# Performance work log

Hardware: AMD Instinct MI355X
Metric: run time of the kernel (lower is better)

The kernel has to match this reference:

```python
import jax, jax.numpy as jnp
import numpy as np
from jax import lax

B, D, S, H, W, T = 128, 512, 30, 14, 14, 12


def setup_inputs() -> dict:
    key = jax.random.key(0)
    ks = jax.random.split(key, 28)
    f = lambda k, shape: jax.random.normal(k, shape, jnp.float32) * 0.05
    return {
        "q": f(ks[0], (B, D)),
        "cws": f(ks[1], (B, D, S)),
        "KB": f(ks[2], (B, D, H, W)),
        "c0": f(ks[3], (B, D)),
        "m0": f(ks[4], (B, D)),
        "Wq": f(ks[5], (D, D)), "bq": f(ks[6], (D,)),
        "Wct": f(ks[7], (2 * D, D)), "bct": f(ks[8], (D,)),
        "wca": f(ks[9], (D,)), "bca": f(ks[10], ()),
        "Wm": f(ks[11], (D, D)), "bm": f(ks[12], (D,)),
        "Wkb": f(ks[13], (D, D)), "bkb": f(ks[14], (D,)),
        "Wrm": f(ks[15], (2 * D, D)), "brm": f(ks[16], (D,)),
        "wra": f(ks[17], (D,)), "bra": f(ks[18], ()),
        "Wwm": f(ks[19], (2 * D, D)), "bwm": f(ks[20], (D,)),
        "wwa": f(ks[21], (D,)), "bwa": f(ks[22], ()),
        "Wam": f(ks[23], (2 * D, D)), "bam": f(ks[24], (D,)),
        "Wg": f(ks[25], (D, D)), "bg": f(ks[26], (D,)),
        "steps": T,
    }


def _mac(q, cws, KB, c0, m0, Wq, bq, Wct, bct, wca, bca, Wm, bm, Wkb, bkb,
         Wrm, brm, wra, bra, Wwm, bwm, wwa, bwa, Wam, bam, Wg, bg, steps):
    b, d, h, w = KB.shape[0], KB.shape[1], KB.shape[2], KB.shape[3]
    KBp = jnp.transpose(KB, (0, 2, 3, 1))          # B,H,W,d
    KB2 = KBp @ Wkb + bkb                           # KB_transform (step-invariant)
    q_i = q @ Wq + bq                               # q_transform (step-invariant)

    nhist = steps + 1
    c_hist = jnp.zeros((nhist, b, d), KB.dtype).at[0].set(c0)
    m_hist = jnp.zeros((nhist, b, d), KB.dtype).at[0].set(m0)

    def step(carry, t):
        c_hist, m_hist, c_prev, m_prev = carry
        # ---- ControlUnit ----
        cq = jnp.concatenate([q_i, c_prev], axis=-1) @ Wct + bct   # B,d
        clog = jnp.einsum('bds,d->bs', cq[:, :, None] * cws, wca) + bca
        cattn = jax.nn.softmax(clog, axis=-1)                       # B,S
        c_i = jnp.einsum('bs,bds->bd', cattn, cws)
        # ---- ReadUnit ----
        mp = m_prev @ Wm + bm                                       # B,d
        I = mp[:, None, None, :] * KB2                              # B,H,W,d
        Im = jnp.concatenate([I, KBp], axis=-1) @ Wrm + brm         # B,H,W,d
        rlog = jnp.einsum('bhwd,d->bhw', c_i[:, None, None, :] * Im, wra) + bra
        rattn = jax.nn.softmax(rlog.reshape(b, -1), axis=-1).reshape(b, h, w)
        m_new = jnp.einsum('bhw,bhwd->bd', rattn, KBp)
        # ---- WriteUnit (self_attn + mem_gate) ----
        _m = jnp.concatenate([m_new, m_prev], axis=-1) @ Wwm + bwm
        slog = jnp.einsum('tbd,d->bt', c_i[None] * c_hist, wwa) + bwa
        valid = jnp.arange(nhist) <= t
        slog = jnp.where(valid[None, :], slog, jnp.float32(-1e9))
        sattn = jax.nn.softmax(slog, axis=-1)                       # B,T+1
        m_sa = jnp.einsum('bt,tbd->bd', sattn, m_hist)
        _m = jnp.concatenate([m_sa, _m], axis=-1) @ Wam + bam
        g = jax.nn.sigmoid(c_i @ Wg + bg)
        _m = g * m_prev + (1.0 - g) * _m
        c_hist = c_hist.at[t + 1].set(c_i)
        m_hist = m_hist.at[t + 1].set(_m)
        return (c_hist, m_hist, c_i, _m), None

    (c_hist, m_hist, c_last, m_last), _ = lax.scan(
        step, (c_hist, m_hist, c0, m0), jnp.arange(steps))
    return m_last


def reference(q, cws, KB, c0, m0, Wq, bq, Wct, bct, wca, bca, Wm, bm, Wkb, bkb,
              Wrm, brm, wra, bra, Wwm, bwm, wwa, bwa, Wam, bam, Wg, bg, steps):
    return _mac(q, cws, KB, c0, m0, Wq, bq, Wct, bct, wca, bca, Wm, bm, Wkb, bkb,
                Wrm, brm, wra, bra, Wwm, bwm, wwa, bwa, Wam, bam, Wg, bg, steps)
```

## Files before the change

kernel.cpp:

```cpp
#include <hip/hip_runtime.h>
#include <cstdint>

#define BB 128
#define DD 512
#define SS 30
#define PP 196
#define TT 12
#define BD (BB*DD)

typedef unsigned short ushortT;
typedef unsigned int uintT;

__device__ __forceinline__ float bf2f(ushortT u)
{
    return __uint_as_float(((uintT)u) << 16);
}

struct GDesc {
    const float *A0, *A1;
    const float *W0, *W1;
    const float *bias;
    float *out;
    const float *e1;
    int nparts, epi, mblk, nblk, aux;
};
struct GPack { GDesc d[6]; };

__global__ __launch_bounds__(256)
void gemm4(GPack pk)
{
    GDesc d = pk.d[blockIdx.z];
    if ((int)blockIdx.x >= d.mblk || (int)blockIdx.y >= d.nblk) return;
    const int tid  = threadIdx.x;
    const int lane = tid & 63;
    const int wv   = __builtin_amdgcn_readfirstlane(tid >> 6);

    if (d.epi == 5) {
        int b = blockIdx.x * 4 + blockIdx.y;
        const float* sat = d.W0 + b * 16;
        float a0 = 0.f, a1 = 0.f;
        for (int tp = 0; tp <= d.aux; ++tp) {
            float s = sat[tp];
            const float* mh = d.A0 + (size_t)tp * BD + (size_t)b * DD;
            a0 = fmaf(s, mh[tid], a0);
            a1 = fmaf(s, mh[tid + 256], a1);
        }
        d.out[(size_t)b * DD + tid] = a0;
        d.out[(size_t)b * DD + tid + 256] = a1;
        return;
    }

    const int m0 = blockIdx.x * 4;
    const int c0 = blockIdx.y * 128;
    float accx[4], accy[4];
    #pragma unroll
    for (int m = 0; m < 4; ++m) { accx[m] = 0.f; accy[m] = 0.f; }

    for (int p = 0; p < d.nparts; ++p) {
        const float* A = p ? d.A1 : d.A0;
        const float* W = p ? d.W1 : d.W0;
        const float* a = A + (size_t)m0 * 512 + wv * 128;
        const float2* Wb = (const float2*)(W + (size_t)(wv * 128) * 512 + c0) + lane;
        #pragma unroll 4
        for (int k = 0; k < 128; ++k) {
            float2 w2 = Wb[(size_t)k * 256];
            #pragma unroll
            for (int m = 0; m < 4; ++m) {
                float av = a[m * 512 + k];
                accx[m] = fmaf(av, w2.x, accx[m]);
                accy[m] = fmaf(av, w2.y, accy[m]);
            }
        }
    }

    __shared__ float red[4][4][128];
    #pragma unroll
    for (int m = 0; m < 4; ++m)
        *(float2*)&red[wv][m][lane * 2] = make_float2(accx[m], accy[m]);
    __syncthreads();

    for (int i = tid; i < 512; i += 256) {
        int mm = i >> 7, cl = i & 127;
        float s = (red[0][mm][cl] + red[1][mm][cl])
                + (red[2][mm][cl] + red[3][mm][cl]);
        int row = m0 + mm, col = c0 + cl;
        size_t o = (size_t)row * 512 + col;
        if (d.epi == 0)      d.out[o] = s + d.bias[col];
        else if (d.epi == 1) { float v = s + d.bias[col];
                               d.out[o] = 1.f / (1.f + __expf(-v)); }
        else if (d.epi == 4) d.out[o] = s + d.e1[o];
        else                 d.out[o] = s;
    }
}

struct SP {
    const float *cq, *cws, *cwsT, *wca, *bca, *wra, *wwa, *bwa;
    float *c_hist, *sattn, *vb;
    const float *msa, *mnw, *gb, *b2, *Wam, *WA, *WB;
    float *m_hist, *dst;
    int t;
};

__global__ __launch_bounds__(512)
void stepA(SP P)
{
    const int tid = threadIdx.x;
    const int lane = tid & 63;
    __shared__ float cqw[512], ciw[512];
    __shared__ float clog2[32], cattn[32], slog[16];
    __shared__ float red[8][2][128];

    if ((int)blockIdx.x < 128) {
        if (P.t >= TT) return;
        int b = blockIdx.x, w = tid >> 6, t = P.t;
        cqw[tid] = P.cq[(size_t)b*DD + tid] * P.wca[tid];
        __syncthreads();
        for (int s = w; s < SS; s += 8) {
            const float* row = P.cwsT + ((size_t)b*SS + s)*DD;
            float a = 0.f;
            #pragma unroll
            for (int j = 0; j < 8; ++j)
                a = fmaf(cqw[lane + 64*j], row[lane + 64*j], a);
            for (int off = 32; off; off >>= 1) a += __shfl_xor(a, off, 64);
            if (lane == 0) clog2[s] = a;
        }
        __syncthreads();
        if (tid < 32) {
            float v = (tid < SS) ? clog2[tid] + P.bca[0] : -1e30f;
            float mx = v;
            for (int off = 16; off; off >>= 1) mx = fmaxf(mx, __shfl_xor(mx, off, 32));
            float e = (tid < SS) ? __expf(v - mx) : 0.f;
            float sm = e;
            for (int off = 16; off; off >>= 1) sm += __shfl_xor(sm, off, 32);
            cattn[tid] = e / sm;
        }
        __syncthreads();
        {
            const float* base = P.cws + (size_t)b*DD*SS + (size_t)tid*SS;
            float acc = 0.f;
            #pragma unroll
            for (int j = 0; j < SS; ++j) acc = fmaf(cattn[j], base[j], acc);
            P.c_hist[(size_t)(t+1)*BD + (size_t)b*DD + tid] = acc;
            P.vb[(size_t)b*DD + tid] = acc * P.wra[tid];
            ciw[tid] = acc * P.wwa[tid];
        }
        __syncthreads();
        for (int tp = tid >> 6; tp <= t; tp += 8) {
            const float* ch = P.c_hist + (size_t)tp*BD + (size_t)b*DD;
            float a = 0.f;
            #pragma unroll
            for (int j = 0; j < 8; ++j)
                a = fmaf(ciw[lane + 64*j], ch[lane + 64*j], a);
            for (int off = 32; off; off >>= 1) a += __shfl_xor(a, off, 64);
            if (lane == 0) slog[tp] = a;
        }
        __syncthreads();
        if (tid < 16) {
            float v = (tid <= t) ? slog[tid] + P.bwa[0] : -1e30f;
            float mx = v;
            for (int off = 8; off; off >>= 1) mx = fmaxf(mx, __shfl_xor(mx, off, 16));
            float e = (tid <= t) ? __expf(v - mx) : 0.f;
            float sm = e;
            for (int off = 8; off; off >>= 1) sm += __shfl_xor(sm, off, 16);
            P.sattn[b*16 + tid] = e / sm;
        }
    } else {
        if (P.t == 0) return;
        int gb_ = blockIdx.x - 128;
        int mt = gb_ >> 2, nc = gb_ & 3;
        int wv = __builtin_amdgcn_readfirstlane(tid >> 6);
        const int koff = wv * 64;
        const float* mprev = P.m_hist + (size_t)(P.t - 1) * BD;
        const int r0 = mt * 2;
        float ax0 = 0.f, ay0 = 0.f, ax1 = 0.f, ay1 = 0.f;

        {
            const float* a = P.msa + (size_t)r0 * 512 + koff;
            const float2* Wb = (const float2*)(P.Wam + (size_t)koff * 512 + nc * 128) + lane;
            #pragma unroll 8
            for (int k = 0; k < 64; ++k) {
                float2 w2 = Wb[(size_t)k * 256];
                float av0 = a[k], av1 = a[512 + k];
                ax0 = fmaf(av0, w2.x, ax0); ay0 = fmaf(av0, w2.y, ay0);
                ax1 = fmaf(av1, w2.x, ax1); ay1 = fmaf(av1, w2.y, ay1);
            }
        }
        {
            const float* a = P.mnw + (size_t)r0 * 512 + koff;
            const float2* Wb = (const float2*)(P.WA + (size_t)koff * 512 + nc * 128) + lane;
            #pragma unroll 8
            for (int k = 0; k < 64; ++k) {
                float2 w2 = Wb[(size_t)k * 256];
                float av0 = a[k], av1 = a[512 + k];
                ax0 = fmaf(av0, w2.x, ax0); ay0 = fmaf(av0, w2.y, ay0);
                ax1 = fmaf(av1, w2.x, ax1); ay1 = fmaf(av1, w2.y, ay1);
            }
        }
        {
            const float* a = mprev + (size_t)r0 * 512 + koff;
            const float2* Wb = (const float2*)(P.WB + (size_t)koff * 512 + nc * 128) + lane;
            #pragma unroll 8
            for (int k = 0; k < 64; ++k) {
                float2 w2 = Wb[(size_t)k * 256];
                float av0 = a[k], av1 = a[512 + k];
                ax0 = fmaf(av0, w2.x, ax0); ay0 = fmaf(av0, w2.y, ay0);
                ax1 = fmaf(av1, w2.x, ax1); ay1 = fmaf(av1, w2.y, ay1);
            }
        }
        *(float2*)&red[wv][0][lane*2] = make_float2(ax0, ay0);
        *(float2*)&red[wv][1][lane*2] = make_float2(ax1, ay1);
        __syncthreads();
        if (tid < 256) {
            int mm = tid >> 7, cl = tid & 127;
            float s = 0.f;
            #pragma unroll
            for (int j = 0; j < 8; ++j) s += red[j][mm][cl];
            int row = r0 + mm, col = nc*128 + cl;
            size_t o = (size_t)row*512 + col;
            float v = s + P.b2[col];
            float g = P.gb[o];
            float pv = mprev[o];
            P.dst[o] = g*pv + (1.f - g)*v;
        }
    }
}

__global__ __launch_bounds__(256)
void read1y(const ushortT* __restrict__ KBh, const float* __restrict__ ubuf,
            const float* __restrict__ mp, const float* __restrict__ WkbT,
            const float* __restrict__ vW, float* __restrict__ rlogp)
{
    int b = blockIdx.x, dg = blockIdx.y, tid = threadIdx.x;
    int lane = tid & 63, w = tid >> 6;
    __shared__ float red[4][64];
    __shared__ float yb[64];
    {
        const float* ur = ubuf + (size_t)b*512;
        const float* mr = mp + (size_t)b*512;
        const float* Wc = WkbT + dg*64 + lane;
        float s = 0.f;
        for (int k = w*128; k < w*128 + 128; ++k)
            s = fmaf(ur[k]*mr[k], Wc[(size_t)k*512], s);
        red[w][lane] = s;
    }
    __syncthreads();
    if (tid < 64)
        yb[tid] = (red[0][tid]+red[1][tid]) + (red[2][tid]+red[3][tid])
                + vW[(size_t)b*512 + dg*64 + tid];
    __syncthreads();
    float a0=0.f, a1=0.f, a2=0.f, a3=0.f;
    if (tid < PP) {
        const ushortT* kb = KBh + ((size_t)b*512 + dg*64)*PP + tid;
        #pragma unroll 4
        for (int dd = 0; dd < 64; dd += 4) {
            a0 = fmaf(bf2f(kb[(size_t)(dd+0)*PP]), yb[dd+0], a0);
            a1 = fmaf(bf2f(kb[(size_t)(dd+1)*PP]), yb[dd+1], a1);
            a2 = fmaf(bf2f(kb[(size_t)(dd+2)*PP]), yb[dd+2], a2);
            a3 = fmaf(bf2f(kb[(size_t)(dd+3)*PP]), yb[dd+3], a3);
        }
    }
    rlogp[((size_t)b*8 + dg)*256 + tid] = (a0+a1)+(a2+a3);
}

__global__ __launch_bounds__(256)
void read2(const ushortT* __restrict__ KBh, const float* __restrict__ rlogp,
           float* __restrict__ m_new)
{
    int b = blockIdx.x, dg = blockIdx.y;
    int tid = threadIdx.x, lane = tid & 63, w = tid >> 6;
    __shared__ float ex[256];
    __shared__ float wred[4];

    float v = -1e30f;
    if (tid < PP) {
        const float* rp = rlogp + (size_t)b*2048 + tid;
        float t0 = rp[0]    + rp[256];
        float t1 = rp[512]  + rp[768];
        float t2 = rp[1024] + rp[1280];
        float t3 = rp[1536] + rp[1792];
        v = (t0+t1)+(t2+t3);
    }
    float mx = v;
    for (int off = 32; off; off >>= 1) mx = fmaxf(mx, __shfl_xor(mx, off, 64));
    if (lane == 0) wred[w] = mx;
    __syncthreads();
    float gmax = fmaxf(fmaxf(wred[0], wred[1]), fmaxf(wred[2], wred[3]));
    float e = (tid < PP) ? __expf(v - gmax) : 0.f;
    float sm = e;
    for (int off = 32; off; off >>= 1) sm += __shfl_xor(sm, off, 64);
    __syncthreads();
    if (lane == 0) wred[w] = sm;
    __syncthreads();
    float inv = 1.f / ((wred[0]+wred[1]) + (wred[2]+wred[3]));
    ex[tid] = e * inv;
    __syncthreads();

    #pragma unroll 2
    for (int i = 0; i < 16; ++i) {
        int d = dg*64 + w*16 + i;
        const ushortT* row = KBh + ((size_t)b*512 + d)*PP;
        float a = ex[lane]       * bf2f(row[lane])
                + ex[lane + 64]  * bf2f(row[lane + 64])
                + ex[lane + 128] * bf2f(row[lane + 128]);
        if (lane < PP - 192) a = fmaf(ex[lane + 192], bf2f(row[lane + 192]), a);
        for (int off = 32; off; off >>= 1) a += __shfl_xor(a, off, 64);
        if (lane == 0) m_new[(size_t)b*512 + d] = a;
    }
}

__global__ __launch_bounds__(256)
void transpose3(const float* __restrict__ Wrm, const float* __restrict__ Wkb,
                float* __restrict__ WrmTu, float* __restrict__ WrmTv,
                float* __restrict__ WkbT)
{
    const float* src = (blockIdx.z == 0) ? Wrm
                     : (blockIdx.z == 1) ? (Wrm + 512*512) : Wkb;
    float* dst = (blockIdx.z == 0) ? WrmTu : (blockIdx.z == 1) ? WrmTv : WkbT;
    __shared__ float tile[32][33];
    int bx = blockIdx.x*32, by = blockIdx.y*32;
    int tx = threadIdx.x & 31, ty = threadIdx.x >> 5;
    #pragma unroll
    for (int i = 0; i < 32; i += 8)
        tile[ty+i][tx] = src[(size_t)(by+ty+i)*512 + bx+tx];
    __syncthreads();
    #pragma unroll
    for (int i = 0; i < 32; i += 8)
        dst[(size_t)(bx+ty+i)*512 + by+tx] = tile[tx][ty+i];
}

__global__ __launch_bounds__(256)
void transpose_cws(const float* __restrict__ cws, float* __restrict__ cwsT)
{
    int b = blockIdx.x, dc = blockIdx.y;
    __shared__ float tile[32][33];
    int tid = threadIdx.x;
    const float* src = cws + ((size_t)b*DD + dc*32) * SS;
    for (int i = tid; i < 1024; i += 256) {
        int r = i >> 5, s = i & 31;
        if (s < SS) tile[r][s] = src[(size_t)r*SS + s];
    }
    __syncthreads();
    for (int i = tid; i < 1024; i += 256) {
        int s = i >> 5, r = i & 31;
        if (s < SS)
            cwsT[((size_t)b*SS + s)*DD + dc*32 + r] = tile[r][s];
    }
}

__global__ __launch_bounds__(256)
void kb_convert(const float* __restrict__ KB, ushortT* __restrict__ KBh)
{
    size_t i = ((size_t)blockIdx.x * 256 + threadIdx.x) * 8;
    #pragma unroll
    for (int j = 0; j < 8; ++j) {
        uintT bits = __float_as_uint(KB[i + j]);
        uintT r = (bits + 0x7FFFu + ((bits >> 16) & 1u)) >> 16;
        KBh[i + j] = (ushortT)r;
    }
}

__global__ __launch_bounds__(256)
void vecmat(const float* __restrict__ v, const float* __restrict__ W,
            const float* __restrict__ bias, float* __restrict__ out)
{
    int lane = threadIdx.x & 63, w = threadIdx.x >> 6;
    int n = blockIdx.x * 64 + lane;
    float s = 0.f;
    for (int k = w*128; k < w*128 + 128; ++k)
        s = fmaf(v[k], W[(size_t)k*512 + n], s);
    __shared__ float red[4][64];
    red[w][lane] = s;
    __syncthreads();
    if (threadIdx.x < 64) {
        int nn = blockIdx.x * 64 + threadIdx.x;
        out[nn] = red[0][threadIdx.x] + red[1][threadIdx.x]
                + red[2][threadIdx.x] + red[3][threadIdx.x] + bias[nn];
    }
}

__global__ __launch_bounds__(256)
void init_hist(const float* __restrict__ c0, const float* __restrict__ m0,
               float* __restrict__ c_hist, float* __restrict__ m_hist)
{
    int i = blockIdx.x * 256 + threadIdx.x;
    if (i < BD) { c_hist[i] = c0[i]; m_hist[i] = m0[i]; }
}

extern "C" void kernel_launch(void* const* d_in, const int* in_sizes, int n_in,
                              void* d_out, int out_size, void* d_ws, size_t ws_size,
                              hipStream_t stream)
{
    (void)in_sizes; (void)n_in; (void)out_size; (void)ws_size;
    const float* q   = (const float*)d_in[0];
    const float* cws = (const float*)d_in[1];
    const float* KB  = (const float*)d_in[2];
    const float* c0  = (const float*)d_in[3];
    const float* m0  = (const float*)d_in[4];
    const float* Wq  = (const float*)d_in[5];
    const float* bq  = (const float*)d_in[6];
    const float* Wct = (const float*)d_in[7];
    const float* bct = (const float*)d_in[8];
    const float* wca = (const float*)d_in[9];
    const float* bca = (const float*)d_in[10];
    const float* Wm  = (const float*)d_in[11];
    const float* bm  = (const float*)d_in[12];
    const float* Wkb = (const float*)d_in[13];
    const float* Wrm = (const float*)d_in[15];
    const float* wra = (const float*)d_in[17];
    const float* Wwm = (const float*)d_in[19];
    const float* bwm = (const float*)d_in[20];
    const float* wwa = (const float*)d_in[21];
    const float* bwa = (const float*)d_in[22];
    const float* Wam = (const float*)d_in[23];
    const float* bam = (const float*)d_in[24];
    const float* Wg  = (const float*)d_in[25];
    const float* bg  = (const float*)d_in[26];

    float* ws      = (float*)d_ws;
    float* c_hist  = ws;
    float* m_hist  = ws + 13*BD;
    float* qct     = ws + 26*BD;
    float* q_i     = ws + 27*BD;
    float* cq      = ws + 28*BD;
    float* mp      = ws + 29*BD;
    float* vb      = ws + 30*BD;
    float* ubuf    = ws + 31*BD;
    float* vW      = ws + 32*BD;
    float* gb      = ws + 33*BD;
    float* msa     = ws + 34*BD;
    float* mnw     = ws + 35*BD;
    float* sattn   = ws + 36*BD;
    float* rlogp   = ws + 37*BD;
    float* WrmTu   = ws + 41*BD;
    float* WrmTv   = ws + 45*BD;
    float* WkbT    = ws + 49*BD;
    float* WA      = ws + 53*BD;
    float* WB      = ws + 57*BD;
    float* b2      = ws + 61*BD;
    float* cwsT    = ws + 62*BD;
    ushortT* KBh   = (ushortT*)(ws + 92*BD);

    const float* Wct_bot = Wct + 512*512;
    const float* Wam_bot = Wam + 512*512;
    const float* Wwm_bot = Wwm + 512*512;
    dim3 blk(256);
    GDesc Z = { nullptr,nullptr,nullptr,nullptr,nullptr,nullptr,nullptr,
                1, 6, 0, 0, 0 };

    transpose3<<<dim3(16,16,3), blk, 0, stream>>>(Wrm, Wkb, WrmTu, WrmTv, WkbT);
    transpose_cws<<<dim3(128,16), blk, 0, stream>>>(cws, cwsT);
    kb_convert<<<dim3(6272), blk, 0, stream>>>(KB, KBh);
    init_hist<<<dim3(BD/256), blk, 0, stream>>>(c0, m0, c_hist, m_hist);
    {
        GPack pk;
        pk.d[0] = { Wwm, nullptr, Wam_bot, nullptr, nullptr, WA, nullptr,
                    1, 6, 128, 4, 0 };
        pk.d[1] = { Wwm_bot, nullptr, Wam_bot, nullptr, nullptr, WB, nullptr,
                    1, 6, 128, 4, 0 };
        pk.d[2] = { q, nullptr, Wq, nullptr, bq, q_i, nullptr,
                    1, 0, 32, 4, 0 };
        pk.d[3] = Z; pk.d[4] = Z; pk.d[5] = Z;
        gemm4<<<dim3(128,4,3), blk, 0, stream>>>(pk);
    }
    {
        GPack pk;
        pk.d[0] = { q_i, nullptr, Wct, nullptr, bct, qct, nullptr,
                    1, 0, 32, 4, 0 };
        pk.d[1] = { q_i, c0, Wct, Wct_bot, bct, cq, nullptr,
                    2, 0, 32, 4, 0 };
        pk.d[2] = Z; pk.d[3] = Z; pk.d[4] = Z; pk.d[5] = Z;
        gemm4<<<dim3(32,4,2), blk, 0, stream>>>(pk);
    }
    vecmat<<<dim3(8), blk, 0, stream>>>(bwm, Wam_bot, bam, b2);

    for (int t = 0; t <= TT; ++t) {
        {
            SP P;
            P.cq = cq; P.cws = cws; P.cwsT = cwsT;
            P.wca = wca; P.bca = bca; P.wra = wra; P.wwa = wwa; P.bwa = bwa;
            P.c_hist = c_hist; P.sattn = sattn; P.vb = vb;
            P.msa = msa; P.mnw = mnw; P.gb = gb; P.b2 = b2;
            P.Wam = Wam; P.WA = WA; P.WB = WB;
            P.m_hist = m_hist;
            P.dst = (t == TT) ? (float*)d_out : (m_hist + (size_t)t * BD);
            P.t = t;
            stepA<<<dim3(384), dim3(512), 0, stream>>>(P);
        }
        if (t == TT) break;

        float* c_i = c_hist + (size_t)(t+1) * BD;
        {
            GPack pk;
            pk.d[0] = { vb, nullptr, WrmTu, nullptr, nullptr, ubuf, nullptr,
                        1, 6, 32, 4, 0 };
            pk.d[1] = { vb, nullptr, WrmTv, nullptr, nullptr, vW, nullptr,
                        1, 6, 32, 4, 0 };
            pk.d[2] = { c_i, nullptr, Wg, nullptr, bg, gb, nullptr,
                        1, 1, 32, 4, 0 };
            pk.d[3] = { c_i, nullptr, Wct_bot, nullptr, nullptr, cq, qct,
                        1, 4, 32, 4, 0 };
            pk.d[4] = { m_hist + (size_t)t * BD, nullptr, Wm, nullptr, bm, mp,
                        nullptr, 1, 0, 32, 4, 0 };
            pk.d[5] = { m_hist, nullptr, sattn, nullptr, nullptr, msa, nullptr,
                        1, 5, 32, 4, t };
            gemm4<<<dim3(32,4,6), blk, 0, stream>>>(pk);
        }
        read1y<<<dim3(BB,8), blk, 0, stream>>>(KBh, ubuf, mp, WkbT, vW, rlogp);
        read2<<<dim3(BB,8), blk, 0, stream>>>(KBh, rlogp, mnw);
    }
}
```

Measured before the change: 793.8 us.

## Fuse read kernels with grid barrier, merge setup kernels, widen GEMM row tiles

Merges read1y and read2 into one kernel that waits on a per-batch atomic counter, so each batch's 8 blocks can reach the softmax/read phase without a second launch. Folds the setup kernels (transposes, bf16 conversion, history init, bias vecmat) into a single launch. Doubles rows per block in gemm4 and stepA's GEMM path, halving grid sizes and improving weight reuse. The trade-offs are fewer blocks and less parallelism, plus the spin-wait, which relies on all 8 blocks of a batch being co-resident to avoid deadlock.

```diff
diff --git a/kernel.cpp b/kernel.cpp
--- a/kernel.cpp
+++ b/kernel.cpp
@@ -36,25 +36,28 @@
     const int wv   = __builtin_amdgcn_readfirstlane(tid >> 6);
 
     if (d.epi == 5) {
-        int b = blockIdx.x * 4 + blockIdx.y;
-        const float* sat = d.W0 + b * 16;
-        float a0 = 0.f, a1 = 0.f;
-        for (int tp = 0; tp <= d.aux; ++tp) {
-            float s = sat[tp];
-            const float* mh = d.A0 + (size_t)tp * BD + (size_t)b * DD;
-            a0 = fmaf(s, mh[tid], a0);
-            a1 = fmaf(s, mh[tid + 256], a1);
-        }
-        d.out[(size_t)b * DD + tid] = a0;
-        d.out[(size_t)b * DD + tid + 256] = a1;
+        int bb = (blockIdx.x * 4 + blockIdx.y) * 2;
+        #pragma unroll
+        for (int b = bb; b < bb + 2; ++b) {
+            const float* sat = d.W0 + b * 16;
+            float a0 = 0.f, a1 = 0.f;
+            for (int tp = 0; tp <= d.aux; ++tp) {
+                float s = sat[tp];
+                const float* mh = d.A0 + (size_t)tp * BD + (size_t)b * DD;
+                a0 = fmaf(s, mh[tid], a0);
+                a1 = fmaf(s, mh[tid + 256], a1);
+            }
+            d.out[(size_t)b * DD + tid] = a0;
+            d.out[(size_t)b * DD + tid + 256] = a1;
+        }
         return;
     }
 
-    const int m0 = blockIdx.x * 4;
+    const int m0 = blockIdx.x * 8;
     const int c0 = blockIdx.y * 128;
-    float accx[4], accy[4];
+    float accx[8], accy[8];
     #pragma unroll
-    for (int m = 0; m < 4; ++m) { accx[m] = 0.f; accy[m] = 0.f; }
+    for (int m = 0; m < 8; ++m) { accx[m] = 0.f; accy[m] = 0.f; }
 
     for (int p = 0; p < d.nparts; ++p) {
         const float* A = p ? d.A1 : d.A0;
@@ -65,7 +68,7 @@
         for (int k = 0; k < 128; ++k) {
             float2 w2 = Wb[(size_t)k * 256];
             #pragma unroll
-            for (int m = 0; m < 4; ++m) {
+            for (int m = 0; m < 8; ++m) {
                 float av = a[m * 512 + k];
                 accx[m] = fmaf(av, w2.x, accx[m]);
                 accy[m] = fmaf(av, w2.y, accy[m]);
@@ -73,13 +76,13 @@
         }
     }
 
-    __shared__ float red[4][4][128];
+    __shared__ float red[4][8][128];
     #pragma unroll
-    for (int m = 0; m < 4; ++m)
+    for (int m = 0; m < 8; ++m)
         *(float2*)&red[wv][m][lane * 2] = make_float2(accx[m], accy[m]);
     __syncthreads();
 
-    for (int i = tid; i < 512; i += 256) {
+    for (int i = tid; i < 1024; i += 256) {
         int mm = i >> 7, cl = i & 127;
         float s = (red[0][mm][cl] + red[1][mm][cl])
                 + (red[2][mm][cl] + red[3][mm][cl]);
@@ -108,7 +111,7 @@
     const int lane = tid & 63;
     __shared__ float cqw[512], ciw[512];
     __shared__ float clog2[32], cattn[32], slog[16];
-    __shared__ float red[8][2][128];
+    __shared__ float red[8][4][128];
 
     if ((int)blockIdx.x < 128) {
         if (P.t >= TT) return;
@@ -171,46 +174,53 @@
         int wv = __builtin_amdgcn_readfirstlane(tid >> 6);
         const int koff = wv * 64;
         const float* mprev = P.m_hist + (size_t)(P.t - 1) * BD;
-        const int r0 = mt * 2;
-        float ax0 = 0.f, ay0 = 0.f, ax1 = 0.f, ay1 = 0.f;
+        const int r0 = mt * 4;
+        float ax[4] = {0.f,0.f,0.f,0.f}, ay[4] = {0.f,0.f,0.f,0.f};
 
         {
             const float* a = P.msa + (size_t)r0 * 512 + koff;
             const float2* Wb = (const float2*)(P.Wam + (size_t)koff * 512 + nc * 128) + lane;
-            #pragma unroll 8
+            #pragma unroll 4
             for (int k = 0; k < 64; ++k) {
                 float2 w2 = Wb[(size_t)k * 256];
-                float av0 = a[k], av1 = a[512 + k];
-                ax0 = fmaf(av0, w2.x, ax0); ay0 = fmaf(av0, w2.y, ay0);
-                ax1 = fmaf(av1, w2.x, ax1); ay1 = fmaf(av1, w2.y, ay1);
+                #pragma unroll
+                for (int m = 0; m < 4; ++m) {
+                    float av = a[m*512 + k];
+                    ax[m] = fmaf(av, w2.x, ax[m]); ay[m] = fmaf(av, w2.y, ay[m]);
+                }
             }
         }
         {
             const float* a = P.mnw + (size_t)r0 * 512 + koff;
             const float2* Wb = (const float2*)(P.WA + (size_t)koff * 512 + nc * 128) + lane;
-            #pragma unroll 8
+            #pragma unroll 4
             for (int k = 0; k < 64; ++k) {
                 float2 w2 = Wb[(size_t)k * 256];
-                float av0 = a[k], av1 = a[512 + k];
-                ax0 = fmaf(av0, w2.x, ax0); ay0 = fmaf(av0, w2.y, ay0);
-                ax1 = fmaf(av1, w2.x, ax1); ay1 = fmaf(av1, w2.y, ay1);
+                #pragma unroll
+                for (int m = 0; m < 4; ++m) {
+                    float av = a[m*512 + k];
+                    ax[m] = fmaf(av, w2.x, ax[m]); ay[m] = fmaf(av, w2.y, ay[m]);
+                }
             }
         }
         {
             const float* a = mprev + (size_t)r0 * 512 + koff;
             const float2* Wb = (const float2*)(P.WB + (size_t)koff * 512 + nc * 128) + lane;
-            #pragma unroll 8
+            #pragma unroll 4
             for (int k = 0; k < 64; ++k) {
                 float2 w2 = Wb[(size_t)k * 256];
-                float av0 = a[k], av1 = a[512 + k];
-                ax0 = fmaf(av0, w2.x, ax0); ay0 = fmaf(av0, w2.y, ay0);
-                ax1 = fmaf(av1, w2.x, ax1); ay1 = fmaf(av1, w2.y, ay1);
+                #pragma unroll
+                for (int m = 0; m < 4; ++m) {
+                    float av = a[m*512 + k];
+                    ax[m] = fmaf(av, w2.x, ax[m]); ay[m] = fmaf(av, w2.y, ay[m]);
+                }
             }
         }
-        *(float2*)&red[wv][0][lane*2] = make_float2(ax0, ay0);
-        *(float2*)&red[wv][1][lane*2] = make_float2(ax1, ay1);
-        __syncthreads();
-        if (tid < 256) {
+        #pragma unroll
+        for (int m = 0; m < 4; ++m)
+            *(float2*)&red[wv][m][lane*2] = make_float2(ax[m], ay[m]);
+        __syncthreads();
+        {
             int mm = tid >> 7, cl = tid & 127;
             float s = 0.f;
             #pragma unroll
@@ -226,14 +236,18 @@
 }
 
 __global__ __launch_bounds__(256)
-void read1y(const ushortT* __restrict__ KBh, const float* __restrict__ ubuf,
-            const float* __restrict__ mp, const float* __restrict__ WkbT,
-            const float* __restrict__ vW, float* __restrict__ rlogp)
+void readfused(const ushortT* __restrict__ KBh, const float* __restrict__ ubuf,
+               const float* __restrict__ mp, const float* __restrict__ WkbT,
+               const float* __restrict__ vW, float* __restrict__ rlogp,
+               float* __restrict__ m_new, int* __restrict__ rcnt, int t)
 {
     int b = blockIdx.x, dg = blockIdx.y, tid = threadIdx.x;
     int lane = tid & 63, w = tid >> 6;
     __shared__ float red[4][64];
     __shared__ float yb[64];
+    __shared__ float ex[256];
+    __shared__ float wred[4];
+
     {
         const float* ur = ubuf + (size_t)b*512;
         const float* mr = mp + (size_t)b*512;
@@ -248,28 +262,31 @@
         yb[tid] = (red[0][tid]+red[1][tid]) + (red[2][tid]+red[3][tid])
                 + vW[(size_t)b*512 + dg*64 + tid];
     __syncthreads();
-    float a0=0.f, a1=0.f, a2=0.f, a3=0.f;
-    if (tid < PP) {
-        const ushortT* kb = KBh + ((size_t)b*512 + dg*64)*PP + tid;
-        #pragma unroll 4
-        for (int dd = 0; dd < 64; dd += 4) {
-            a0 = fmaf(bf2f(kb[(size_t)(dd+0)*PP]), yb[dd+0], a0);
-            a1 = fmaf(bf2f(kb[(size_t)(dd+1)*PP]), yb[dd+1], a1);
-            a2 = fmaf(bf2f(kb[(size_t)(dd+2)*PP]), yb[dd+2], a2);
-            a3 = fmaf(bf2f(kb[(size_t)(dd+3)*PP]), yb[dd+3], a3);
-        }
-    }
-    rlogp[((size_t)b*8 + dg)*256 + tid] = (a0+a1)+(a2+a3);
-}
-
-__global__ __launch_bounds__(256)
-void read2(const ushortT* __restrict__ KBh, const float* __restrict__ rlogp,
-           float* __restrict__ m_new)
-{
-    int b = blockIdx.x, dg = blockIdx.y;
-    int tid = threadIdx.x, lane = tid & 63, w = tid >> 6;
-    __shared__ float ex[256];
-    __shared__ float wred[4];
+    {
+        float a0=0.f, a1=0.f, a2=0.f, a3=0.f;
+        if (tid < PP) {
+            const ushortT* kb = KBh + ((size_t)b*512 + dg*64)*PP + tid;
+            #pragma unroll 4
+            for (int dd = 0; dd < 64; dd += 4) {
+                a0 = fmaf(bf2f(kb[(size_t)(dd+0)*PP]), yb[dd+0], a0);
+                a1 = fmaf(bf2f(kb[(size_t)(dd+1)*PP]), yb[dd+1], a1);
+                a2 = fmaf(bf2f(kb[(size_t)(dd+2)*PP]), yb[dd+2], a2);
+                a3 = fmaf(bf2f(kb[(size_t)(dd+3)*PP]), yb[dd+3], a3);
+            }
+        }
+        rlogp[((size_t)b*8 + dg)*256 + tid] = (a0+a1)+(a2+a3);
+    }
+
+    __syncthreads();
+    if (tid == 0) {
+        int* c = rcnt + t*128 + b;
+        __threadfence();
+        __hip_atomic_fetch_add(c, 1, __ATOMIC_ACQ_REL, __HIP_MEMORY_SCOPE_AGENT);
+        while (__hip_atomic_load(c, __ATOMIC_ACQUIRE, __HIP_MEMORY_SCOPE_AGENT) < 8)
+            __builtin_amdgcn_s_sleep(2);
+        __threadfence();
+    }
+    __syncthreads();
 
     float v = -1e30f;
     if (tid < PP) {
@@ -308,82 +325,73 @@
     }
 }
 
+struct SetupP {
+    const float *Wrm, *Wkb, *cws, *KB, *c0v, *m0v, *bwm, *Wam_bot, *bam;
+    float *WrmTu, *WrmTv, *WkbT, *cwsT, *c_hist, *m_hist, *b2;
+    ushortT *KBh;
+};
+
 __global__ __launch_bounds__(256)
-void transpose3(const float* __restrict__ Wrm, const float* __restrict__ Wkb,
-                float* __restrict__ WrmTu, float* __restrict__ WrmTv,
-                float* __restrict__ WkbT)
+void setup_misc(SetupP P)
 {
-    const float* src = (blockIdx.z == 0) ? Wrm
-                     : (blockIdx.z == 1) ? (Wrm + 512*512) : Wkb;
-    float* dst = (blockIdx.z == 0) ? WrmTu : (blockIdx.z == 1) ? WrmTv : WkbT;
     __shared__ float tile[32][33];
-    int bx = blockIdx.x*32, by = blockIdx.y*32;
-    int tx = threadIdx.x & 31, ty = threadIdx.x >> 5;
-    #pragma unroll
-    for (int i = 0; i < 32; i += 8)
-        tile[ty+i][tx] = src[(size_t)(by+ty+i)*512 + bx+tx];
-    __syncthreads();
-    #pragma unroll
-    for (int i = 0; i < 32; i += 8)
-        dst[(size_t)(bx+ty+i)*512 + by+tx] = tile[tx][ty+i];
-}
-
-__global__ __launch_bounds__(256)
-void transpose_cws(const float* __restrict__ cws, float* __restrict__ cwsT)
-{
-    int b = blockIdx.x, dc = blockIdx.y;
-    __shared__ float tile[32][33];
-    int tid = threadIdx.x;
-    const float* src = cws + ((size_t)b*DD + dc*32) * SS;
-    for (int i = tid; i < 1024; i += 256) {
-        int r = i >> 5, s = i & 31;
-        if (s < SS) tile[r][s] = src[(size_t)r*SS + s];
-    }
-    __syncthreads();
-    for (int i = tid; i < 1024; i += 256) {
-        int s = i >> 5, r = i & 31;
-        if (s < SS)
-            cwsT[((size_t)b*SS + s)*DD + dc*32 + r] = tile[r][s];
-    }
-}
-
-__global__ __launch_bounds__(256)
-void kb_convert(const float* __restrict__ KB, ushortT* __restrict__ KBh)
-{
-    size_t i = ((size_t)blockIdx.x * 256 + threadIdx.x) * 8;
-    #pragma unroll
-    for (int j = 0; j < 8; ++j) {
-        uintT bits = __float_as_uint(KB[i + j]);
-        uintT r = (bits + 0x7FFFu + ((bits >> 16) & 1u)) >> 16;
-        KBh[i + j] = (ushortT)r;
-    }
-}
-
-__global__ __launch_bounds__(256)
-void vecmat(const float* __restrict__ v, const float* __restrict__ W,
-            const float* __restrict__ bias, float* __restrict__ out)
-{
-    int lane = threadIdx.x & 63, w = threadIdx.x >> 6;
-    int n = blockIdx.x * 64 + lane;
-    float s = 0.f;
-    for (int k = w*128; k < w*128 + 128; ++k)
-        s = fmaf(v[k], W[(size_t)k*512 + n], s);
-    __shared__ float red[4][64];
-    red[w][lane] = s;
-    __syncthreads();
-    if (threadIdx.x < 64) {
-        int nn = blockIdx.x * 64 + threadIdx.x;
-        out[nn] = red[0][threadIdx.x] + red[1][threadIdx.x]
-                + red[2][threadIdx.x] + red[3][threadIdx.x] + bias[nn];
-    }
-}
-
-__global__ __launch_bounds__(256)
-void init_hist(const float* __restrict__ c0, const float* __restrict__ m0,
-               float* __restrict__ c_hist, float* __restrict__ m_hist)
-{
-    int i = blockIdx.x * 256 + threadIdx.x;
-    if (i < BD) { c_hist[i] = c0[i]; m_hist[i] = m0[i]; }
+    int id = blockIdx.x, tid = threadIdx.x;
+
+    if (id < 768) {
+        int which = id >> 8, tj = id & 255;
+        const float* src = (which == 0) ? P.Wrm
+                         : (which == 1) ? (P.Wrm + 512*512) : P.Wkb;
+        float* dst = (which == 0) ? P.WrmTu : (which == 1) ? P.WrmTv : P.WkbT;
+        int bx = (tj & 15) * 32, by = (tj >> 4) * 32;
+        int tx = tid & 31, ty = tid >> 5;
+        #pragma unroll
+        for (int i = 0; i < 32; i += 8)
+            tile[ty+i][tx] = src[(size_t)(by+ty+i)*512 + bx+tx];
+        __syncthreads();
+        #pragma unroll
+        for (int i = 0; i < 32; i += 8)
+            dst[(size_t)(bx+ty+i)*512 + by+tx] = tile[tx][ty+i];
+    } else if (id < 2816) {
+        int j = id - 768;
+        int b = j >> 4, dc = j & 15;
+        const float* src = P.cws + ((size_t)b*DD + dc*32) * SS;
+        for (int i = tid; i < 1024; i += 256) {
+            int r = i >> 5, s = i & 31;
+            if (s < SS) tile[r][s] = src[(size_t)r*SS + s];
+        }
+        __syncthreads();
+        for (int i = tid; i < 1024; i += 256) {
+            int s = i >> 5, r = i & 31;
+            if (s < SS)
+                P.cwsT[((size_t)b*SS + s)*DD + dc*32 + r] = tile[r][s];
+        }
+    } else if (id < 9088) {
+        size_t i = ((size_t)(id - 2816) * 256 + tid) * 8;
+        #pragma unroll
+        for (int j = 0; j < 8; ++j) {
+            uintT bits = __float_as_uint(P.KB[i + j]);
+            uintT r = (bits + 0x7FFFu + ((bits >> 16) & 1u)) >> 16;
+            P.KBh[i + j] = (ushortT)r;
+        }
+    } else if (id < 9344) {
+        int i = (id - 9088) * 256 + tid;
+        P.c_hist[i] = P.c0v[i];
+        P.m_hist[i] = P.m0v[i];
+    } else {
+        int lane = tid & 63, w = tid >> 6;
+        int n = (id - 9344) * 64 + lane;
+        float s = 0.f;
+        for (int k = w*128; k < w*128 + 128; ++k)
+            s = fmaf(P.bwm[k], P.Wam_bot[(size_t)k*512 + n], s);
+        __shared__ float red[4][64];
+        red[w][lane] = s;
+        __syncthreads();
+        if (tid < 64) {
+            int nn = (id - 9344) * 64 + tid;
+            P.b2[nn] = red[0][tid] + red[1][tid] + red[2][tid] + red[3][tid]
+                     + P.bam[nn];
+        }
+    }
 }
 
 extern "C" void kernel_launch(void* const* d_in, const int* in_sizes, int n_in,
@@ -439,6 +447,7 @@
     float* b2      = ws + 61*BD;
     float* cwsT    = ws + 62*BD;
     ushortT* KBh   = (ushortT*)(ws + 92*BD);
+    int* rcnt      = (int*)(ws + 190*BD);
 
     const float* Wct_bot = Wct + 512*512;
     const float* Wam_bot = Wam + 512*512;
@@ -447,31 +456,35 @@
     GDesc Z = { nullptr,nullptr,nullptr,nullptr,nullptr,nullptr,nullptr,
                 1, 6, 0, 0, 0 };
 
-    transpose3<<<dim3(16,16,3), blk, 0, stream>>>(Wrm, Wkb, WrmTu, WrmTv, WkbT);
-    transpose_cws<<<dim3(128,16), blk, 0, stream>>>(cws, cwsT);
-    kb_convert<<<dim3(6272), blk, 0, stream>>>(KB, KBh);
-    init_hist<<<dim3(BD/256), blk, 0, stream>>>(c0, m0, c_hist, m_hist);
+    hipMemsetAsync(rcnt, 0, TT*128*sizeof(int), stream);
+    {
+        SetupP S;
+        S.Wrm = Wrm; S.Wkb = Wkb; S.cws = cws; S.KB = KB;
+        S.c0v = c0; S.m0v = m0; S.bwm = bwm; S.Wam_bot = Wam_bot; S.bam = bam;
+        S.WrmTu = WrmTu; S.WrmTv = WrmTv; S.WkbT = WkbT; S.cwsT = cwsT;
+        S.c_hist = c_hist; S.m_hist = m_hist; S.b2 = b2; S.KBh = KBh;
+        setup_misc<<<dim3(9352), blk, 0, stream>>>(S);
+    }
     {
         GPack pk;
         pk.d[0] = { Wwm, nullptr, Wam_bot, nullptr, nullptr, WA, nullptr,
-                    1, 6, 128, 4, 0 };
+                    1, 6, 64, 4, 0 };
         pk.d[1] = { Wwm_bot, nullptr, Wam_bot, nullptr, nullptr, WB, nullptr,
-                    1, 6, 128, 4, 0 };
+                    1, 6, 64, 4, 0 };
         pk.d[2] = { q, nullptr, Wq, nullptr, bq, q_i, nullptr,
-                    1, 0, 32, 4, 0 };
+                    1, 0, 16, 4, 0 };
         pk.d[3] = Z; pk.d[4] = Z; pk.d[5] = Z;
-        gemm4<<<dim3(128,4,3), blk, 0, stream>>>(pk);
+        gemm4<<<dim3(64,4,3), blk, 0, stream>>>(pk);
     }
     {
         GPack pk;
         pk.d[0] = { q_i, nullptr, Wct, nullptr, bct, qct, nullptr,
-                    1, 0, 32, 4, 0 };
+                    1, 0, 16, 4, 0 };
         pk.d[1] = { q_i, c0, Wct, Wct_bot, bct, cq, nullptr,
-                    2, 0, 32, 4, 0 };
+                    2, 0, 16, 4, 0 };
         pk.d[2] = Z; pk.d[3] = Z; pk.d[4] = Z; pk.d[5] = Z;
-        gemm4<<<dim3(32,4,2), blk, 0, stream>>>(pk);
-    }
-    vecmat<<<dim3(8), blk, 0, stream>>>(bwm, Wam_bot, bam, b2);
+        gemm4<<<dim3(16,4,2), blk, 0, stream>>>(pk);
+    }
 
     for (int t = 0; t <= TT; ++t) {
         {
@@ -484,7 +497,7 @@
             P.m_hist = m_hist;
             P.dst = (t == TT) ? (float*)d_out : (m_hist + (size_t)t * BD);
             P.t = t;
-            stepA<<<dim3(384), dim3(512), 0, stream>>>(P);
+            stepA<<<dim3(256), dim3(512), 0, stream>>>(P);
         }
         if (t == TT) break;
 
@@ -492,20 +505,20 @@
         {
             GPack pk;
             pk.d[0] = { vb, nullptr, WrmTu, nullptr, nullptr, ubuf, nullptr,
-                        1, 6, 32, 4, 0 };
+                        1, 6, 16, 4, 0 };
             pk.d[1] = { vb, nullptr, WrmTv, nullptr, nullptr, vW, nullptr,
-                        1, 6, 32, 4, 0 };
+                        1, 6, 16, 4, 0 };
             pk.d[2] = { c_i, nullptr, Wg, nullptr, bg, gb, nullptr,
-                        1, 1, 32, 4, 0 };
+                        1, 1, 16, 4, 0 };
             pk.d[3] = { c_i, nullptr, Wct_bot, nullptr, nullptr, cq, qct,
-                        1, 4, 32, 4, 0 };
+                        1, 4, 16, 4, 0 };
             pk.d[4] = { m_hist + (size_t)t * BD, nullptr, Wm, nullptr, bm, mp,
-                        nullptr, 1, 0, 32, 4, 0 };
+                        nullptr, 1, 0, 16, 4, 0 };
             pk.d[5] = { m_hist, nullptr, sattn, nullptr, nullptr, msa, nullptr,
-                        1, 5, 32, 4, t };
-            gemm4<<<dim3(32,4,6), blk, 0, stream>>>(pk);
-        }
-        read1y<<<dim3(BB,8), blk, 0, stream>>>(KBh, ubuf, mp, WkbT, vW, rlogp);
-        read2<<<dim3(BB,8), blk, 0, stream>>>(KBh, rlogp, mnw);
+                        1, 5, 16, 4, t };
+            gemm4<<<dim3(16,4,6), blk, 0, stream>>>(pk);
+        }
+        readfused<<<dim3(BB,8), blk, 0, stream>>>(KBh, ubuf, mp, WkbT, vW,
+                                                  rlogp, mnw, rcnt, t);
     }
 }
```

New measurement: 2.266 ms. 2.86x slower.
